# Kernel optimization log

Hardware: AMD Instinct MI355X
Metric: run time of the kernel (lower is better)

## Reference

```python
import jax, jax.numpy as jnp
import numpy as np

# Superlevel-set persistence (sublevel of f = -beta) on a Freudenthal-triangulated grid.
# dim-0 pairs: Kruskal union-find on vertices (edges ascending by lower-star value).
# dim-1 pairs: union-find on the dual graph (triangles + outer face, edges descending),
# valid because the grid complex is a planar disk (standard duality for 2-complexes).

def _find(parent, x):
    root = x
    while parent[root] != root:
        root = parent[root]
    while parent[x] != root:
        parent[x], x = root, parent[x]
    return root

def _persistence_pairs(beta_np):
    n0, n1 = beta_np.shape
    f = (-beta_np).reshape(-1)            # sublevel filtration of -beta == superlevel of beta
    N = n0 * n1
    idx = np.arange(N).reshape(n0, n1)
    # Freudenthal edges: horizontal, vertical, diagonal (i,j)-(i+1,j+1)
    eu = np.concatenate([idx[:, :-1].ravel(), idx[:-1, :].ravel(), idx[:-1, :-1].ravel()])
    ev = np.concatenate([idx[:, 1:].ravel(), idx[1:, :].ravel(), idx[1:, 1:].ravel()])
    e_crit = np.where(f[eu] >= f[ev], eu, ev)   # lower-star critical vertex of each edge
    e_val = f[e_crit]
    # ---- dim 0: union-find over vertices, edges ascending ----
    order = np.argsort(e_val, kind='stable')
    parent = np.arange(N)
    birth_vtx = np.arange(N)              # per-root: vertex of minimal f in component
    b0, d0 = [], []
    for e in order:
        ru, rv = _find(parent, eu[e]), _find(parent, ev[e])
        if ru == rv:
            continue
        if f[birth_vtx[ru]] < f[birth_vtx[rv]]:
            ru, rv = rv, ru               # ru = younger component (larger birth) dies
        b0.append(birth_vtx[ru]); d0.append(e_crit[e])
        parent[ru] = rv                   # surviving root keeps the older birth vertex
    # ---- triangles of the Freudenthal triangulation ----
    t_a = np.concatenate([idx[:-1, :-1].ravel(), idx[:-1, :-1].ravel()])
    t_b = np.concatenate([idx[1:, :-1].ravel(), idx[:-1, 1:].ravel()])
    t_c = np.concatenate([idx[1:, 1:].ravel(), idx[1:, 1:].ravel()])
    T = t_a.shape[0]
    tris = np.stack([t_a, t_b, t_c], 1)
    t_arg = np.argmax(np.stack([f[t_a], f[t_b], f[t_c]], 1), 1)
    t_crit = tris[np.arange(T), t_arg]    # lower-star critical vertex of each triangle
    # ---- dual graph: nodes = triangles + outer face, dual edges = primal edges ----
    edge2face = {}
    for t in range(T):
        vs = tris[t]
        for a, b in ((0, 1), (0, 2), (1, 2)):
            key = (min(vs[a], vs[b]), max(vs[a], vs[b]))
            edge2face.setdefault(key, []).append(t)
    OUTER = T
    du, dv, dval, dcrit = [], [], [], []
    for (a, b), faces in edge2face.items():
        du.append(faces[0]); dv.append(faces[1] if len(faces) > 1 else OUTER)
        c = a if f[a] >= f[b] else b
        dcrit.append(c); dval.append(f[c])
    du = np.array(du); dv = np.array(dv)
    dval = np.array(dval); dcrit = np.array(dcrit)
    # ---- dim 1: union-find over faces, dual edges descending ----
    order1 = np.argsort(-dval, kind='stable')
    parent1 = np.arange(T + 1)
    fval = np.concatenate([f[t_crit], [np.inf]])   # outer face value = +inf
    fcrit = np.concatenate([t_crit, [-1]])
    birth_face = np.arange(T + 1)         # per-root: face of maximal value in component
    be1, dt1 = [], []
    for e in order1:
        ru, rv = _find(parent1, du[e]), _find(parent1, dv[e])
        if ru == rv:
            continue
        if fval[birth_face[ru]] > fval[birth_face[rv]]:
            ru, rv = rv, ru               # ru = younger (smaller max face value)
        be1.append(dcrit[e])              # H1 birth: the merging primal edge
        dt1.append(fcrit[birth_face[ru]]) # H1 death: max triangle of younger component
        parent1[ru] = rv
    return (np.asarray(b0, np.int64), np.asarray(d0, np.int64),
            np.asarray(be1, np.int64), np.asarray(dt1, np.int64))


def setup_inputs() -> dict:
    key = jax.random.key(0)
    beta = jax.random.normal(key, (128, 128), dtype=jnp.float32)
    return {"beta": beta}


def reference(beta):
    b0, d0, be1, dt1 = _persistence_pairs(np.asarray(beta))
    bf = beta.reshape(-1)
    # dim-0 superlevel bar lengths: beta[birth_vtx] - beta[death_vtx]  (SumBarcodeLengths(dim=0))
    loss0 = jnp.sum(bf[b0] - bf[d0]) if b0.size else jnp.zeros((), bf.dtype)
    # dim-1 lengths: beta[edge_crit] - beta[tri_crit]; skip the single longest bar
    if be1.size:
        l1 = bf[be1] - bf[dt1]
        loss1 = jnp.sum(l1) - jnp.max(l1)  # PartialSumBarcodeLengths(dim=1, skip=1)
    else:
        loss1 = jnp.zeros((), bf.dtype)
    return loss1 + loss0
```

## Files before the change

### kernel.cpp

```cpp
#include <hip/hip_runtime.h>

#define NV 16384
#define EH 16256
#define EVV 16256
#define ED 16129
#define NE 48641
#define NT 32258
#define ND 32259
#define OUTERF 32258
#define TAILN 8192
#define FINT 1024

typedef unsigned int u32;
typedef unsigned short u16;

static __host__ __device__ constexpr size_t al256(size_t x) { return (x + 255) & ~(size_t)255; }
static constexpr size_t OFF_ACC   = 0;
static constexpr size_t OFF_R32   = 256;
static constexpr size_t OFF_FVAL  = OFF_R32   + al256(NV * 4);
static constexpr size_t OFF_CTV   = OFF_FVAL  + al256(ND * 4);
static constexpr size_t OFF_CNTR  = OFF_CTV   + al256(NT * 2);
static constexpr size_t OFF_FRK   = OFF_CNTR  + al256(NV * 4);
static constexpr size_t OFF_FRV   = OFF_FRK   + al256(ND * 4);
static constexpr size_t OFF_DVAL  = OFF_FRV   + al256(ND * 4);
static constexpr size_t OFF_WLA   = OFF_DVAL  + al256(NE * 4);
static constexpr size_t OFF_WLB   = OFF_WLA   + al256(NE * 8);
static constexpr size_t OFF_RTS   = OFF_WLB   + al256(NE * 8);
static constexpr size_t OFF_MTG   = OFF_RTS   + al256(NE * 4);
static constexpr size_t OFF_MTG2  = OFF_MTG   + al256((ND + 1) * 4);
static constexpr size_t OFF_PARG  = OFF_MTG2  + al256((ND + 1) * 4);

__device__ __forceinline__ u32 fmap(float x) {
  u32 u = __float_as_uint(x);
  return (u & 0x80000000u) ? ~u : (u | 0x80000000u);
}
__device__ __forceinline__ float funmap(u32 m) {
  u32 u = (m & 0x80000000u) ? (m & 0x7FFFFFFFu) : ~m;
  return __uint_as_float(u);
}

__device__ __forceinline__ int findh(volatile u16* par, int x) {
  while (true) {
    int p = par[x];
    if (p == x) return x;
    int gp = par[p];
    if (gp == p) return p;
    par[x] = (u16)gp;
    x = gp;
  }
}

__device__ __forceinline__ void decode_pe(u32 e, int& eu, int& ev) {
  if (e < EH) { int i = (int)(e / 127u), j = (int)(e - (u32)i * 127u); eu = (i << 7) + j; ev = eu + 1; }
  else if (e < EH + EVV) { int k = (int)(e - EH); eu = k; ev = k + 128; }
  else { int k = (int)(e - EH - EVV); int i = k / 127, j = k - i * 127; eu = (i << 7) + j; ev = eu + 129; }
}
__device__ __forceinline__ void decode_df(u32 e, int& fa, int& fb) {
  if (e < EH) { int i = (int)(e / 127u), j = (int)(e - (u32)i * 127u);
    fa = (i < 127) ? (ED + i * 127 + j) : OUTERF;
    fb = (i >= 1) ? ((i - 1) * 127 + j) : OUTERF; }
  else if (e < EH + EVV) { int k = (int)(e - EH); int i = k >> 7, j = k & 127;
    fa = (j < 127) ? (i * 127 + j) : OUTERF;
    fb = (j >= 1) ? (ED + i * 127 + (j - 1)) : OUTERF; }
  else { int k = (int)(e - EH - EVV); int i = k / 127, j = k - i * 127;
    fa = i * 127 + j; fb = ED + i * 127 + j; }
}

__global__ void k_init(float* accF, u32* r32, u32* mtabG, u32* mtabG2, u32* parG32) {
  int i = blockIdx.x * 256 + threadIdx.x;
  if (i < 12) accF[i] = 0.f;
  if (i < NV) r32[i] = 0u;
  if (i < (ND + 1) / 2) parG32[i] = ((2u * (u32)i + 1u) << 16) | (2u * (u32)i);
  if (i < ND + 1) { mtabG[i] = 0xFFFFFFFFu; mtabG2[i] = 0xFFFFFFFFu; }
}

__global__ void k_rankv(const float* __restrict__ beta, u32* r32) {
  int v = blockIdx.x * 256 + threadIdx.x;
  int c = blockIdx.y;
  float bv = beta[v];
  int u0 = c << 10;
  int cnt = 0;
#pragma unroll 8
  for (int u = u0; u < u0 + 1024; ++u) {
    float bu = beta[u];
    cnt += (bu < bv || (bu == bv && u < v)) ? 1 : 0;
  }
  if (cnt) atomicAdd(&r32[v], (u32)cnt);
}

__global__ void k_build(const float* __restrict__ beta, const u32* __restrict__ r32,
                        float* fval, u16* ctv, float* accF, u32* accU) {
  __shared__ float ls[4], lm[4];
  int bid = blockIdx.x, tid = threadIdx.x;
  if (bid < 64) {
    int v = (bid << 8) + tid;
    float b = beta[v];
    float s = b, m = b;
    for (int off = 32; off >= 1; off >>= 1) {
      s += __shfl_down(s, off);
      m = fmaxf(m, __shfl_down(m, off));
    }
    int wid = tid >> 6;
    if ((tid & 63) == 0) { ls[wid] = s; lm[wid] = m; }
    __syncthreads();
    if (tid == 0) {
      s = ls[0] + ls[1] + ls[2] + ls[3];
      m = fmaxf(fmaxf(lm[0], lm[1]), fmaxf(lm[2], lm[3]));
      atomicAdd(&accF[1], s);
      atomicMax(&accU[2], fmap(m));
    }
  } else {
    int t = ((bid - 64) << 8) + tid;
    float c = 0.f;
    if (t < NT) {
      int i, j, v0, v1, v2;
      if (t < ED) { i = t / 127; j = t - i * 127; v0 = (i << 7) + j; v1 = v0 + 128; v2 = v0 + 129; }
      else { int u = t - ED; i = u / 127; j = u - i * 127; v0 = (i << 7) + j; v1 = v0 + 1; v2 = v0 + 129; }
      u32 r0 = r32[v0], r1 = r32[v1], r2 = r32[v2];
      int crit = v0; u32 rm = r0;
      if (r1 < rm) { rm = r1; crit = v1; }
      if (r2 < rm) { rm = r2; crit = v2; }
      float fv = -beta[crit];
      fval[t] = fv;
      ctv[t] = (u16)crit;
      c = fv;
      if (t == 0) fval[OUTERF] = __builtin_inff();
    }
    for (int off = 32; off >= 1; off >>= 1) c += __shfl_down(c, off);
    int wid = tid >> 6;
    if ((tid & 63) == 0) ls[wid] = c;
    __syncthreads();
    if (tid == 0) atomicAdd(&accF[3], ls[0] + ls[1] + ls[2] + ls[3]);
  }
}

__global__ void k_cntface(const u16* __restrict__ ctv, const u32* __restrict__ r32, u32* cntR) {
  int v = blockIdx.x * 256 + threadIdx.x;
  int i = v >> 7, j = v & 127;
  int cnt = 0;
  if (i < 127 && j < 127) cnt += (ctv[i * 127 + j] == v);
  if (i >= 1 && j < 127)  cnt += (ctv[(i - 1) * 127 + j] == v);
  if (i >= 1 && j >= 1)   cnt += (ctv[(i - 1) * 127 + (j - 1)] == v);
  if (i < 127 && j < 127) cnt += (ctv[ED + i * 127 + j] == v);
  if (i < 127 && j >= 1)  cnt += (ctv[ED + i * 127 + (j - 1)] == v);
  if (i >= 1 && j >= 1)   cnt += (ctv[ED + (i - 1) * 127 + (j - 1)] == v);
  cntR[r32[v]] = (u32)cnt;
}

__global__ __launch_bounds__(1024) void k_scanR(u32* cntR) {
  __shared__ u32 wsum[16];
  int tid = threadIdx.x;
  u32 loc[16]; u32 s = 0;
#pragma unroll
  for (int k = 0; k < 16; ++k) { u32 c = cntR[(tid << 4) + k]; loc[k] = s; s += c; }
  int lane = tid & 63, wid = tid >> 6;
  u32 incl = s;
  for (int off = 1; off < 64; off <<= 1) {
    u32 o = __shfl_up(incl, off);
    if (lane >= off) incl += o;
  }
  if (lane == 63) wsum[wid] = incl;
  __syncthreads();
  u32 wbase = 0;
  for (int w = 0; w < wid; ++w) wbase += wsum[w];
  u32 base = wbase + incl - s + 1;
#pragma unroll
  for (int k = 0; k < 16; ++k) cntR[(tid << 4) + k] = base + loc[k];
}

__global__ void k_facerank(const u16* __restrict__ ctv, const u32* __restrict__ r32,
                           const u32* __restrict__ startsR, const float* __restrict__ fval,
                           u32* frk, float* frv) {
  int g = blockIdx.x * 256 + threadIdx.x;
  if (g == 0) { frk[OUTERF] = 0u; frv[0] = __builtin_inff(); }
  if (g >= NT) return;
  int v = ctv[g];
  int i = v >> 7, j = v & 127;
  int local = 0, f;
  if (i < 127 && j < 127) { f = i * 127 + j;             local += (f < g && ctv[f] == v); }
  if (i >= 1 && j < 127)  { f = (i - 1) * 127 + j;       local += (f < g && ctv[f] == v); }
  if (i >= 1 && j >= 1)   { f = (i - 1) * 127 + (j - 1); local += (f < g && ctv[f] == v); }
  if (i < 127 && j < 127) { f = ED + i * 127 + j;        local += (f < g && ctv[f] == v); }
  if (i < 127 && j >= 1)  { f = ED + i * 127 + (j - 1);  local += (f < g && ctv[f] == v); }
  if (i >= 1 && j >= 1)   { f = ED + (i - 1) * 127 + (j - 1); local += (f < g && ctv[f] == v); }
  u32 rk = startsR[r32[v]] + (u32)local;
  frk[g] = rk;
  frv[rk] = fval[g];
}

__global__ void k_edges(const float* __restrict__ beta, const u32* __restrict__ r32,
                        const u32* __restrict__ frk,
                        float* dvals, uint2* wl0, float* accF, u32* mtabG) {
  int e = blockIdx.x * 256 + threadIdx.x;
  float dv = 0.f;
  if (e < NE) {
    int eu, ev; decode_pe((u32)e, eu, ev);
    int fa, fb; decode_df((u32)e, fa, fb);
    u32 ru = r32[eu], rv = r32[ev];
    u32 rr = min(ru, rv);
    int cv = (ru <= rv) ? eu : ev;
    dv = -beta[cv];
    dvals[e] = dv;
    u32 ra = frk[fa], rb = frk[fb];
    u32 key = (rr << 17) | (u32)e;
    wl0[e] = make_uint2(ra | (rb << 16), key);
    atomicMin(&mtabG[ra], key);
    atomicMin(&mtabG[rb], key);
  }
  float ds = dv;
  for (int off = 32; off >= 1; off >>= 1) ds += __shfl_down(ds, off);
  if ((threadIdx.x & 63) == 0) atomicAdd(&accF[0], ds);
}

__global__ void k_win0(const uint2* __restrict__ wl0, const float* __restrict__ dvals,
                       const float* __restrict__ frv, const u32* __restrict__ mtabG,
                       u16* parG, uint2* owl, float* accF, u32* accU) {
  __shared__ float ls[4], lm[4];
  int tid = threadIdx.x, lane = tid & 63;
  int e = blockIdx.x * 256 + tid;
  float wDl = 0.f, lmx = 0.f;
  bool surv = false;
  uint2 rec = make_uint2(0u, 0u);
  if (e < NE) {
    rec = wl0[e];
    u32 a = rec.x & 0xFFFFu, b = rec.x >> 16;
    u32 y = max(a, b), o = min(a, b);
    if (mtabG[y] == rec.y) {
      parG[y] = (u16)o;
      float dv = dvals[rec.y & 0x1FFFFu];
      wDl = dv;
      lmx = frv[y] - dv;
    } else {
      surv = true;
    }
  }
  unsigned long long mk = __ballot(surv);
  int base = 0;
  if (lane == 0) {
    int c = __popcll(mk);
    if (c) base = (int)atomicAdd(&accU[6], (u32)c);
  }
  base = __shfl(base, 0);
  if (surv) owl[base + __popcll(mk & ((1ull << lane) - 1ull))] = rec;
  for (int off = 32; off >= 1; off >>= 1) {
    wDl += __shfl_down(wDl, off);
    lmx = fmaxf(lmx, __shfl_down(lmx, off));
  }
  if (lane == 0) { ls[tid >> 6] = wDl; lm[tid >> 6] = lmx; }
  __syncthreads();
  if (tid == 0) {
    float s = ls[0] + ls[1] + ls[2] + ls[3];
    float m = fmaxf(fmaxf(lm[0], lm[1]), fmaxf(lm[2], lm[3]));
    atomicAdd(&accF[4], s);
    atomicMax(&accU[5], fmap(m));
  }
}

__global__ void k_claimN(const uint2* __restrict__ wl, u16* parG, u32* rts,
                         u32* mtab, const u32* __restrict__ accU, int ci) {
  int n1 = (int)accU[ci];
  int i = blockIdx.x * 256 + threadIdx.x;
  if (i >= n1) return;
  uint2 rec = wl[i];
  int ra = findh((volatile u16*)parG, (int)(rec.x & 0xFFFFu));
  int rb = findh((volatile u16*)parG, (int)(rec.x >> 16));
  if (ra == rb) {
    rts[i] = 0xFFFFFFFFu;
  } else {
    rts[i] = (u32)ra | ((u32)rb << 16);
    atomicMin(&mtab[ra], rec.y);
    atomicMin(&mtab[rb], rec.y);
  }
}

__global__ void k_winN(const uint2* __restrict__ wl, const u32* __restrict__ rts,
                       const float* __restrict__ dvals, const float* __restrict__ frv,
                       const u32* __restrict__ mtab, u16* parG, uint2* owl,
                       float* accF, u32* accU, int ci, int co) {
  __shared__ float ls[4], lm[4];
  int tid = threadIdx.x, lane = tid & 63;
  int n1 = (int)accU[ci];
  int i = blockIdx.x * 256 + tid;
  bool active = i < n1;
  float wDl = 0.f, lmx = 0.f;
  bool surv = false;
  u32 pr = 0xFFFFFFFFu, key = 0;
  if (active) {
    key = wl[i].y;
    pr = rts[i];
  }
  if (active && pr != 0xFFFFFFFFu) {
    u32 a = pr & 0xFFFFu, b = pr >> 16;
    u32 y = max(a, b), o = min(a, b);
    if (mtab[y] == key) {
      parG[y] = (u16)o;
      float dv = dvals[key & 0x1FFFFu];
      wDl = dv;
      lmx = frv[y] - dv;
    } else {
      surv = true;
    }
  }
  unsigned long long mk = __ballot(surv);
  int base = 0;
  if (lane == 0) {
    int c = __popcll(mk);
    if (c) base = (int)atomicAdd(&accU[co], (u32)c);
  }
  base = __shfl(base, 0);
  if (surv) owl[base + __popcll(mk & ((1ull << lane) - 1ull))] = make_uint2(pr, key);
  for (int off = 32; off >= 1; off >>= 1) {
    wDl += __shfl_down(wDl, off);
    lmx = fmaxf(lmx, __shfl_down(lmx, off));
  }
  if (lane == 0) { ls[tid >> 6] = wDl; lm[tid >> 6] = lmx; }
  __syncthreads();
  if (tid == 0) {
    float s = ls[0] + ls[1] + ls[2] + ls[3];
    float m = fmaxf(fmaxf(lm[0], lm[1]), fmaxf(lm[2], lm[3]));
    atomicAdd(&accF[4], s);
    atomicMax(&accU[5], fmap(m));
  }
}

__global__ __launch_bounds__(1024) void k_dual(
    uint2* __restrict__ wlA, uint2* __restrict__ wlB, u32* __restrict__ rts,
    const u32* __restrict__ parG32, const float* __restrict__ dvals,
    const float* __restrict__ frv,
    const float* __restrict__ accF, const u32* __restrict__ accU, float* out) {
  __shared__ u16 par[ND + 1];
  __shared__ u32 pool[24576];
  __shared__ int nCur, nNxt;
  __shared__ int nTail[2];
  __shared__ float redS[16], redM[16];
  int tid = threadIdx.x, lane = tid & 63;
  {
    u32* p32 = (u32*)par;
    for (int v = tid; v < (ND + 1) / 2; v += 1024) p32[v] = parG32[v];
  }
  for (int h = tid; h < 16384; h += 1024) pool[h] = 0xFFFFFFFFu;
  if (tid == 0) { nNxt = 0; nTail[0] = 0; nTail[1] = 0; nCur = (int)accU[9]; }
  float wD = 0.f, lmax = 0.f;
  __syncthreads();
  uint2* cur = wlA;
  uint2* nxt = wlB;
  int n = nCur;
  for (int round = 0; round < 50000 && n > TAILN; ++round) {
    for (int i0 = 0; i0 < n; i0 += 1024) {
      int i = i0 + tid;
      if (i < n) {
        uint2 rec = cur[i];
        int ra = findh((volatile u16*)par, (int)(rec.x & 0xFFFFu));
        int rb = findh((volatile u16*)par, (int)(rec.x >> 16));
        if (ra == rb) {
          rts[i] = 0xFFFFFFFFu;
        } else {
          rts[i] = (u32)ra | ((u32)rb << 16);
          atomicMin(&pool[(u32)ra & 16383u], rec.y);
          atomicMin(&pool[(u32)rb & 16383u], rec.y);
        }
      }
    }
    __syncthreads();
    for (int i0 = 0; i0 < n; i0 += 1024) {
      int i = i0 + tid;
      bool active = i < n;
      u32 pr = 0xFFFFFFFFu, key = 0;
      if (active) {
        key = cur[i].y;
        pr = rts[i];
      }
      bool pend = active && (pr != 0xFFFFFFFFu);
      u32 y = 0, o = 0;
      bool win = false;
      if (pend) {
        u32 a = pr & 0xFFFFu, b = pr >> 16;
        y = max(a, b); o = min(a, b);
        win = (pool[y & 16383u] == key);
      }
      if (win) {
        par[y] = (u16)o;
        float dv = dvals[key & 0x1FFFFu];
        wD += dv;
        lmax = fmaxf(lmax, frv[y] - dv);
      }
      bool req = pend && !win;
      unsigned long long mk = __ballot(req);
      int base = 0;
      if (lane == 0) {
        int c = __popcll(mk);
        if (c) base = atomicAdd(&nNxt, c);
      }
      base = __shfl(base, 0);
      if (req) {
        int pos = base + __popcll(mk & ((1ull << lane) - 1ull));
        nxt[pos] = make_uint2(pr, key);
      }
    }
    __syncthreads();
    if (n <= 6144) {
      for (int i0 = 0; i0 < n; i0 += 1024) {
        int i = i0 + tid;
        if (i < n) {
          u32 pr = rts[i];
          if (pr != 0xFFFFFFFFu) {
            pool[(pr & 0xFFFFu) & 16383u] = 0xFFFFFFFFu;
            pool[(pr >> 16) & 16383u] = 0xFFFFFFFFu;
          }
        }
      }
    } else {
      for (int h = tid; h < 16384; h += 1024) pool[h] = 0xFFFFFFFFu;
    }
    for (int v = tid; v < ND; v += 1024) {
      int p = par[v]; int pp = par[p];
      if (p != pp) par[v] = (u16)pp;
    }
    if (tid == 0) { nCur = nNxt; nNxt = 0; }
    __syncthreads();
    n = nCur;
    uint2* s = cur; cur = nxt; nxt = s;
  }
  if (n > 0) {
    uint2* wlL = (uint2*)(pool + 8192);
    for (int i = tid; i < n; i += 1024) wlL[i] = cur[i];
    __syncthreads();
    int nL = n;
    int cb = 0;
    u32 oldp[8];
#pragma unroll
    for (int k = 0; k < 8; ++k) oldp[k] = 0xFFFFFFFFu;
    for (int sr = 0; sr < 100000; ++sr) {
      if (nL <= FINT) break;
      u32* mtC = pool + (cb << 12);
      u32* mtO = pool + ((cb ^ 1) << 12);
      u32 prc[8], keyr[8];
#pragma unroll
      for (int k = 0; k < 8; ++k) {
        if (oldp[k] != 0xFFFFFFFFu) {
          mtO[(oldp[k] & 0xFFFFu) & 4095u] = 0xFFFFFFFFu;
          mtO[(oldp[k] >> 16) & 4095u] = 0xFFFFFFFFu;
        }
        prc[k] = 0xFFFFFFFFu; keyr[k] = 0u;
        int i = tid + (k << 10);
        if (i < nL) {
          uint2 rec = wlL[i];
          int ra = findh((volatile u16*)par, (int)(rec.x & 0xFFFFu));
          int rb = findh((volatile u16*)par, (int)(rec.x >> 16));
          if (ra != rb) {
            u32 pr = (u32)ra | ((u32)rb << 16);
            prc[k] = pr; keyr[k] = rec.y;
            atomicMin(&mtC[(u32)ra & 4095u], rec.y);
            atomicMin(&mtC[(u32)rb & 4095u], rec.y);
          }
        }
      }
      if (tid == 0) nTail[cb] = 0;
      __syncthreads();
#pragma unroll
      for (int k = 0; k < 8; ++k) {
        bool surv = false;
        if (prc[k] != 0xFFFFFFFFu) {
          u32 a = prc[k] & 0xFFFFu, b = prc[k] >> 16;
          u32 y = max(a, b), o = min(a, b);
          if (mtC[y & 4095u] == keyr[k]) {
            par[y] = (u16)o;
            float dv = dvals[keyr[k] & 0x1FFFFu];
            wD += dv;
            lmax = fmaxf(lmax, frv[y] - dv);
          } else {
            surv = true;
          }
        }
        unsigned long long mk = __ballot(surv);
        int base = 0;
        if (lane == 0) {
          int c = __popcll(mk);
          if (c) base = atomicAdd(&nTail[cb], c);
        }
        base = __shfl(base, 0);
        if (surv) {
          int pos = base + __popcll(mk & ((1ull << lane) - 1ull));
          wlL[pos] = make_uint2(prc[k], keyr[k]);
        }
        oldp[k] = prc[k];
      }
      __syncthreads();
      nL = nTail[cb];
      cb ^= 1;
    }
    for (int h = tid; h < 8192; h += 1024) pool[h] = 0xFFFFFFFFu;
    __syncthreads();
    if (nL > 0 && tid < 64) {
      int m = nL;
      int mm = m;
      int guard = 0;
      while (mm > 0 && guard++ < 100000) {
        u32 prc[16];
        int resolved = 0;
#pragma unroll
        for (int k = 0; k < 16; ++k) {
          prc[k] = 0xFFFFFFFFu;
          int i = (k << 6) + lane;
          if (i < m) {
            uint2 rec = wlL[i];
            if (rec.x != 0xFFFFFFFFu) {
              int ra = findh((volatile u16*)par, (int)(rec.x & 0xFFFFu));
              int rb = findh((volatile u16*)par, (int)(rec.x >> 16));
              if (ra == rb) {
                wlL[i].x = 0xFFFFFFFFu;
                resolved++;
              } else {
                u32 pr = (u32)ra | ((u32)rb << 16);
                prc[k] = pr;
                wlL[i].x = pr;
                atomicMin(&pool[(u32)ra & 4095u], rec.y);
                atomicMin(&pool[(u32)rb & 4095u], rec.y);
              }
            }
          }
        }
        asm volatile("s_waitcnt lgkmcnt(0)" ::: "memory");
#pragma unroll
        for (int k = 0; k < 16; ++k) {
          if (prc[k] != 0xFFFFFFFFu) {
            int i = (k << 6) + lane;
            u32 key = wlL[i].y;
            u32 a = prc[k] & 0xFFFFu, b = prc[k] >> 16;
            u32 y = max(a, b), o = min(a, b);
            if (pool[y & 4095u] == key) {
              par[y] = (u16)o;
              float dv = dvals[key & 0x1FFFFu];
              wD += dv;
              lmax = fmaxf(lmax, frv[y] - dv);
              wlL[i].x = 0xFFFFFFFFu;
              resolved++;
            }
          }
        }
        asm volatile("s_waitcnt lgkmcnt(0)" ::: "memory");
#pragma unroll
        for (int k = 0; k < 16; ++k) {
          if (prc[k] != 0xFFFFFFFFu) {
            pool[(prc[k] & 0xFFFFu) & 4095u] = 0xFFFFFFFFu;
            pool[(prc[k] >> 16) & 4095u] = 0xFFFFFFFFu;
          }
        }
        asm volatile("s_waitcnt lgkmcnt(0)" ::: "memory");
        for (int off = 32; off >= 1; off >>= 1) resolved += __shfl_down(resolved, off);
        resolved = __shfl(resolved, 0);
        mm -= resolved;
      }
    }
  }
  __syncthreads();
  for (int off = 32; off >= 1; off >>= 1) {
    wD += __shfl_down(wD, off);
    lmax = fmaxf(lmax, __shfl_down(lmax, off));
  }
  if (lane == 0) { redS[tid >> 6] = wD; redM[tid >> 6] = lmax; }
  __syncthreads();
  if (tid == 0) {
    float s = 0.f, m = 0.f;
    for (int w = 0; w < 16; ++w) { s += redS[w]; m = fmaxf(m, redM[w]); }
    s += accF[4];
    m = fmaxf(m, funmap(accU[5]));
    float wmst = accF[0] - s;
    float loss0 = wmst + accF[1] - funmap(accU[2]);
    float sum1 = accF[3] - s;
    out[0] = loss0 + sum1 - m;
  }
}

extern "C" void kernel_launch(void* const* d_in, const int* in_sizes, int n_in,
                              void* d_out, int out_size, void* d_ws, size_t ws_size,
                              hipStream_t stream) {
  const float* beta = (const float*)d_in[0];
  float* out = (float*)d_out;
  char* ws = (char*)d_ws;
  float* accF = (float*)(ws + OFF_ACC);
  u32*   accU = (u32*)(ws + OFF_ACC);
  u32* r32 = (u32*)(ws + OFF_R32);
  float* fval = (float*)(ws + OFF_FVAL);
  u16* ctv = (u16*)(ws + OFF_CTV);
  u32* cntR = (u32*)(ws + OFF_CNTR);
  u32* frk = (u32*)(ws + OFF_FRK);
  float* frv = (float*)(ws + OFF_FRV);
  float* dvals = (float*)(ws + OFF_DVAL);
  uint2* wlA = (uint2*)(ws + OFF_WLA);
  uint2* wlB = (uint2*)(ws + OFF_WLB);
  u32* rts = (u32*)(ws + OFF_RTS);
  u32* mtabG = (u32*)(ws + OFF_MTG);
  u32* mtabG2 = (u32*)(ws + OFF_MTG2);
  u16* parG = (u16*)(ws + OFF_PARG);
  u32* parG32 = (u32*)(ws + OFF_PARG);

  hipLaunchKernelGGL(k_init, dim3(127), dim3(256), 0, stream, accF, r32, mtabG, mtabG2, parG32);
  hipLaunchKernelGGL(k_rankv, dim3(64, 16), dim3(256), 0, stream, beta, r32);
  hipLaunchKernelGGL(k_build, dim3(191), dim3(256), 0, stream, beta, r32, fval, ctv, accF, accU);
  hipLaunchKernelGGL(k_cntface, dim3(64), dim3(256), 0, stream, ctv, r32, cntR);
  hipLaunchKernelGGL(k_scanR, dim3(1), dim3(1024), 0, stream, cntR);
  hipLaunchKernelGGL(k_facerank, dim3(127), dim3(256), 0, stream, ctv, r32, cntR, fval, frk, frv);
  hipLaunchKernelGGL(k_edges, dim3(191), dim3(256), 0, stream, beta, r32, frk, dvals, wlA, accF, mtabG);
  hipLaunchKernelGGL(k_win0, dim3(191), dim3(256), 0, stream, wlA, dvals, frv, mtabG, parG, wlB, accF, accU);
  hipMemsetAsync(mtabG, 0xFF, (ND + 1) * sizeof(u32), stream);
  hipLaunchKernelGGL(k_claimN, dim3(191), dim3(256), 0, stream, wlB, parG, rts, mtabG2, accU, 6);
  hipLaunchKernelGGL(k_winN, dim3(191), dim3(256), 0, stream, wlB, rts, dvals, frv, mtabG2, parG, wlA, accF, accU, 6, 7);
  hipMemsetAsync(mtabG2, 0xFF, (ND + 1) * sizeof(u32), stream);
  hipLaunchKernelGGL(k_claimN, dim3(191), dim3(256), 0, stream, wlA, parG, rts, mtabG, accU, 7);
  hipLaunchKernelGGL(k_winN, dim3(191), dim3(256), 0, stream, wlA, rts, dvals, frv, mtabG, parG, wlB, accF, accU, 7, 8);
  hipLaunchKernelGGL(k_claimN, dim3(191), dim3(256), 0, stream, wlB, parG, rts, mtabG2, accU, 8);
  hipLaunchKernelGGL(k_winN, dim3(191), dim3(256), 0, stream, wlB, rts, dvals, frv, mtabG2, parG, wlA, accF, accU, 8, 9);
  hipLaunchKernelGGL(k_dual, dim3(1), dim3(1024), 0, stream, wlA, wlB, rts, parG32, dvals, frv, accF, accU, out);
}
```

Before: 257.5 us.

## Fuse mid-pipeline kernels into one cooperative kernel with grid syncs

Replaces the chain of about a dozen small launches and two memsets (build, face counting, scan, face ranking, edge setup, the initial win pass and three claim/win rounds) with a single cooperative kernel of 191 blocks that separates phases with grid.sync. The memsets of the min tables are replaced by targeted resets of only the entries touched in earlier rounds. A second rts buffer is added so consecutive rounds do not overwrite each other's data. This aims to remove per-launch overhead and inter-kernel gaps, at the cost of grid-barrier latency and a single-block scan that now handles 64 elements per thread.

```diff
diff --git a/kernel.cpp b/kernel.cpp
--- a/kernel.cpp
+++ b/kernel.cpp
@@ -1,4 +1,7 @@
 #include <hip/hip_runtime.h>
+#include <hip/hip_cooperative_groups.h>
+
+namespace cg = cooperative_groups;
 
 #define NV 16384
 #define EH 16256
@@ -26,7 +29,8 @@
 static constexpr size_t OFF_WLA   = OFF_DVAL  + al256(NE * 4);
 static constexpr size_t OFF_WLB   = OFF_WLA   + al256(NE * 8);
 static constexpr size_t OFF_RTS   = OFF_WLB   + al256(NE * 8);
-static constexpr size_t OFF_MTG   = OFF_RTS   + al256(NE * 4);
+static constexpr size_t OFF_RTS2  = OFF_RTS   + al256(NE * 4);
+static constexpr size_t OFF_MTG   = OFF_RTS2  + al256(NE * 4);
 static constexpr size_t OFF_MTG2  = OFF_MTG   + al256((ND + 1) * 4);
 static constexpr size_t OFF_PARG  = OFF_MTG2  + al256((ND + 1) * 4);
 
@@ -88,10 +92,18 @@
   if (cnt) atomicAdd(&r32[v], (u32)cnt);
 }
 
-__global__ void k_build(const float* __restrict__ beta, const u32* __restrict__ r32,
-                        float* fval, u16* ctv, float* accF, u32* accU) {
+__global__ __launch_bounds__(256) void k_coop(
+    const float* __restrict__ beta, const u32* __restrict__ r32,
+    float* accF, u32* accU,
+    float* fval, u16* ctv, u32* cntR, u32* frk, float* frv,
+    float* dvals, uint2* wlA, uint2* wlB, u32* rts, u32* rts2,
+    u32* mtabG, u32* mtabG2, u16* parG) {
+  cg::grid_group grid = cg::this_grid();
   __shared__ float ls[4], lm[4];
-  int bid = blockIdx.x, tid = threadIdx.x;
+  __shared__ u32 wsum[4];
+  int tid = threadIdx.x, lane = tid & 63, wid = tid >> 6;
+  int bid = blockIdx.x;
+  int gtid = bid * 256 + tid;
   if (bid < 64) {
     int v = (bid << 8) + tid;
     float b = beta[v];
@@ -100,8 +112,7 @@
       s += __shfl_down(s, off);
       m = fmaxf(m, __shfl_down(m, off));
     }
-    int wid = tid >> 6;
-    if ((tid & 63) == 0) { ls[wid] = s; lm[wid] = m; }
+    if (lane == 0) { ls[wid] = s; lm[wid] = m; }
     __syncthreads();
     if (tid == 0) {
       s = ls[0] + ls[1] + ls[2] + ls[3];
@@ -127,199 +138,199 @@
       if (t == 0) fval[OUTERF] = __builtin_inff();
     }
     for (int off = 32; off >= 1; off >>= 1) c += __shfl_down(c, off);
-    int wid = tid >> 6;
-    if ((tid & 63) == 0) ls[wid] = c;
+    if (lane == 0) ls[wid] = c;
     __syncthreads();
     if (tid == 0) atomicAdd(&accF[3], ls[0] + ls[1] + ls[2] + ls[3]);
   }
-}
-
-__global__ void k_cntface(const u16* __restrict__ ctv, const u32* __restrict__ r32, u32* cntR) {
-  int v = blockIdx.x * 256 + threadIdx.x;
-  int i = v >> 7, j = v & 127;
-  int cnt = 0;
-  if (i < 127 && j < 127) cnt += (ctv[i * 127 + j] == v);
-  if (i >= 1 && j < 127)  cnt += (ctv[(i - 1) * 127 + j] == v);
-  if (i >= 1 && j >= 1)   cnt += (ctv[(i - 1) * 127 + (j - 1)] == v);
-  if (i < 127 && j < 127) cnt += (ctv[ED + i * 127 + j] == v);
-  if (i < 127 && j >= 1)  cnt += (ctv[ED + i * 127 + (j - 1)] == v);
-  if (i >= 1 && j >= 1)   cnt += (ctv[ED + (i - 1) * 127 + (j - 1)] == v);
-  cntR[r32[v]] = (u32)cnt;
-}
-
-__global__ __launch_bounds__(1024) void k_scanR(u32* cntR) {
-  __shared__ u32 wsum[16];
-  int tid = threadIdx.x;
-  u32 loc[16]; u32 s = 0;
-#pragma unroll
-  for (int k = 0; k < 16; ++k) { u32 c = cntR[(tid << 4) + k]; loc[k] = s; s += c; }
-  int lane = tid & 63, wid = tid >> 6;
-  u32 incl = s;
-  for (int off = 1; off < 64; off <<= 1) {
-    u32 o = __shfl_up(incl, off);
-    if (lane >= off) incl += o;
-  }
-  if (lane == 63) wsum[wid] = incl;
-  __syncthreads();
-  u32 wbase = 0;
-  for (int w = 0; w < wid; ++w) wbase += wsum[w];
-  u32 base = wbase + incl - s + 1;
-#pragma unroll
-  for (int k = 0; k < 16; ++k) cntR[(tid << 4) + k] = base + loc[k];
-}
-
-__global__ void k_facerank(const u16* __restrict__ ctv, const u32* __restrict__ r32,
-                           const u32* __restrict__ startsR, const float* __restrict__ fval,
-                           u32* frk, float* frv) {
-  int g = blockIdx.x * 256 + threadIdx.x;
-  if (g == 0) { frk[OUTERF] = 0u; frv[0] = __builtin_inff(); }
-  if (g >= NT) return;
-  int v = ctv[g];
-  int i = v >> 7, j = v & 127;
-  int local = 0, f;
-  if (i < 127 && j < 127) { f = i * 127 + j;             local += (f < g && ctv[f] == v); }
-  if (i >= 1 && j < 127)  { f = (i - 1) * 127 + j;       local += (f < g && ctv[f] == v); }
-  if (i >= 1 && j >= 1)   { f = (i - 1) * 127 + (j - 1); local += (f < g && ctv[f] == v); }
-  if (i < 127 && j < 127) { f = ED + i * 127 + j;        local += (f < g && ctv[f] == v); }
-  if (i < 127 && j >= 1)  { f = ED + i * 127 + (j - 1);  local += (f < g && ctv[f] == v); }
-  if (i >= 1 && j >= 1)   { f = ED + (i - 1) * 127 + (j - 1); local += (f < g && ctv[f] == v); }
-  u32 rk = startsR[r32[v]] + (u32)local;
-  frk[g] = rk;
-  frv[rk] = fval[g];
-}
-
-__global__ void k_edges(const float* __restrict__ beta, const u32* __restrict__ r32,
-                        const u32* __restrict__ frk,
-                        float* dvals, uint2* wl0, float* accF, u32* mtabG) {
-  int e = blockIdx.x * 256 + threadIdx.x;
-  float dv = 0.f;
-  if (e < NE) {
-    int eu, ev; decode_pe((u32)e, eu, ev);
-    int fa, fb; decode_df((u32)e, fa, fb);
-    u32 ru = r32[eu], rv = r32[ev];
-    u32 rr = min(ru, rv);
-    int cv = (ru <= rv) ? eu : ev;
-    dv = -beta[cv];
-    dvals[e] = dv;
-    u32 ra = frk[fa], rb = frk[fb];
-    u32 key = (rr << 17) | (u32)e;
-    wl0[e] = make_uint2(ra | (rb << 16), key);
-    atomicMin(&mtabG[ra], key);
-    atomicMin(&mtabG[rb], key);
-  }
-  float ds = dv;
-  for (int off = 32; off >= 1; off >>= 1) ds += __shfl_down(ds, off);
-  if ((threadIdx.x & 63) == 0) atomicAdd(&accF[0], ds);
-}
-
-__global__ void k_win0(const uint2* __restrict__ wl0, const float* __restrict__ dvals,
-                       const float* __restrict__ frv, const u32* __restrict__ mtabG,
-                       u16* parG, uint2* owl, float* accF, u32* accU) {
-  __shared__ float ls[4], lm[4];
-  int tid = threadIdx.x, lane = tid & 63;
-  int e = blockIdx.x * 256 + tid;
-  float wDl = 0.f, lmx = 0.f;
-  bool surv = false;
-  uint2 rec = make_uint2(0u, 0u);
-  if (e < NE) {
-    rec = wl0[e];
-    u32 a = rec.x & 0xFFFFu, b = rec.x >> 16;
-    u32 y = max(a, b), o = min(a, b);
-    if (mtabG[y] == rec.y) {
-      parG[y] = (u16)o;
-      float dv = dvals[rec.y & 0x1FFFFu];
-      wDl = dv;
-      lmx = frv[y] - dv;
-    } else {
-      surv = true;
-    }
-  }
-  unsigned long long mk = __ballot(surv);
-  int base = 0;
-  if (lane == 0) {
-    int c = __popcll(mk);
-    if (c) base = (int)atomicAdd(&accU[6], (u32)c);
-  }
-  base = __shfl(base, 0);
-  if (surv) owl[base + __popcll(mk & ((1ull << lane) - 1ull))] = rec;
-  for (int off = 32; off >= 1; off >>= 1) {
-    wDl += __shfl_down(wDl, off);
-    lmx = fmaxf(lmx, __shfl_down(lmx, off));
-  }
-  if (lane == 0) { ls[tid >> 6] = wDl; lm[tid >> 6] = lmx; }
-  __syncthreads();
-  if (tid == 0) {
-    float s = ls[0] + ls[1] + ls[2] + ls[3];
-    float m = fmaxf(fmaxf(lm[0], lm[1]), fmaxf(lm[2], lm[3]));
-    atomicAdd(&accF[4], s);
-    atomicMax(&accU[5], fmap(m));
-  }
-}
-
-__global__ void k_claimN(const uint2* __restrict__ wl, u16* parG, u32* rts,
-                         u32* mtab, const u32* __restrict__ accU, int ci) {
-  int n1 = (int)accU[ci];
-  int i = blockIdx.x * 256 + threadIdx.x;
-  if (i >= n1) return;
-  uint2 rec = wl[i];
-  int ra = findh((volatile u16*)parG, (int)(rec.x & 0xFFFFu));
-  int rb = findh((volatile u16*)parG, (int)(rec.x >> 16));
-  if (ra == rb) {
-    rts[i] = 0xFFFFFFFFu;
-  } else {
-    rts[i] = (u32)ra | ((u32)rb << 16);
-    atomicMin(&mtab[ra], rec.y);
-    atomicMin(&mtab[rb], rec.y);
-  }
-}
-
-__global__ void k_winN(const uint2* __restrict__ wl, const u32* __restrict__ rts,
-                       const float* __restrict__ dvals, const float* __restrict__ frv,
-                       const u32* __restrict__ mtab, u16* parG, uint2* owl,
-                       float* accF, u32* accU, int ci, int co) {
-  __shared__ float ls[4], lm[4];
-  int tid = threadIdx.x, lane = tid & 63;
-  int n1 = (int)accU[ci];
-  int i = blockIdx.x * 256 + tid;
-  bool active = i < n1;
-  float wDl = 0.f, lmx = 0.f;
-  bool surv = false;
-  u32 pr = 0xFFFFFFFFu, key = 0;
-  if (active) {
-    key = wl[i].y;
-    pr = rts[i];
-  }
-  if (active && pr != 0xFFFFFFFFu) {
-    u32 a = pr & 0xFFFFu, b = pr >> 16;
-    u32 y = max(a, b), o = min(a, b);
-    if (mtab[y] == key) {
-      parG[y] = (u16)o;
-      float dv = dvals[key & 0x1FFFFu];
-      wDl = dv;
-      lmx = frv[y] - dv;
-    } else {
-      surv = true;
-    }
-  }
-  unsigned long long mk = __ballot(surv);
-  int base = 0;
-  if (lane == 0) {
-    int c = __popcll(mk);
-    if (c) base = (int)atomicAdd(&accU[co], (u32)c);
-  }
-  base = __shfl(base, 0);
-  if (surv) owl[base + __popcll(mk & ((1ull << lane) - 1ull))] = make_uint2(pr, key);
-  for (int off = 32; off >= 1; off >>= 1) {
-    wDl += __shfl_down(wDl, off);
-    lmx = fmaxf(lmx, __shfl_down(lmx, off));
-  }
-  if (lane == 0) { ls[tid >> 6] = wDl; lm[tid >> 6] = lmx; }
-  __syncthreads();
-  if (tid == 0) {
-    float s = ls[0] + ls[1] + ls[2] + ls[3];
-    float m = fmaxf(fmaxf(lm[0], lm[1]), fmaxf(lm[2], lm[3]));
-    atomicAdd(&accF[4], s);
-    atomicMax(&accU[5], fmap(m));
+  grid.sync();
+  if (gtid < NV) {
+    int v = gtid;
+    int i = v >> 7, j = v & 127;
+    int cnt = 0;
+    if (i < 127 && j < 127) cnt += (ctv[i * 127 + j] == v);
+    if (i >= 1 && j < 127)  cnt += (ctv[(i - 1) * 127 + j] == v);
+    if (i >= 1 && j >= 1)   cnt += (ctv[(i - 1) * 127 + (j - 1)] == v);
+    if (i < 127 && j < 127) cnt += (ctv[ED + i * 127 + j] == v);
+    if (i < 127 && j >= 1)  cnt += (ctv[ED + i * 127 + (j - 1)] == v);
+    if (i >= 1 && j >= 1)   cnt += (ctv[ED + (i - 1) * 127 + (j - 1)] == v);
+    cntR[r32[v]] = (u32)cnt;
+  }
+  grid.sync();
+  if (bid == 0) {
+    int b0 = tid << 6;
+    u32 s = 0;
+    for (int k = 0; k < 64; ++k) s += cntR[b0 + k];
+    u32 incl = s;
+    for (int off = 1; off < 64; off <<= 1) {
+      u32 o = __shfl_up(incl, off);
+      if (lane >= off) incl += o;
+    }
+    if (lane == 63) wsum[wid] = incl;
+    __syncthreads();
+    u32 wbase = 0;
+    for (int w = 0; w < wid; ++w) wbase += wsum[w];
+    u32 running = wbase + incl - s + 1;
+    for (int k = 0; k < 64; ++k) {
+      u32 c = cntR[b0 + k];
+      cntR[b0 + k] = running;
+      running += c;
+    }
+  }
+  grid.sync();
+  if (gtid == 0) { frk[OUTERF] = 0u; frv[0] = __builtin_inff(); }
+  if (gtid < NT) {
+    int g = gtid;
+    int v = ctv[g];
+    int i = v >> 7, j = v & 127;
+    int local = 0, f;
+    if (i < 127 && j < 127) { f = i * 127 + j;             local += (f < g && ctv[f] == v); }
+    if (i >= 1 && j < 127)  { f = (i - 1) * 127 + j;       local += (f < g && ctv[f] == v); }
+    if (i >= 1 && j >= 1)   { f = (i - 1) * 127 + (j - 1); local += (f < g && ctv[f] == v); }
+    if (i < 127 && j < 127) { f = ED + i * 127 + j;        local += (f < g && ctv[f] == v); }
+    if (i < 127 && j >= 1)  { f = ED + i * 127 + (j - 1);  local += (f < g && ctv[f] == v); }
+    if (i >= 1 && j >= 1)   { f = ED + (i - 1) * 127 + (j - 1); local += (f < g && ctv[f] == v); }
+    u32 rk = cntR[r32[v]] + (u32)local;
+    frk[g] = rk;
+    frv[rk] = fval[g];
+  }
+  grid.sync();
+  {
+    int e = gtid;
+    float dv = 0.f;
+    if (e < NE) {
+      int eu, ev; decode_pe((u32)e, eu, ev);
+      int fa, fb; decode_df((u32)e, fa, fb);
+      u32 ru = r32[eu], rv = r32[ev];
+      u32 rr = min(ru, rv);
+      int cv = (ru <= rv) ? eu : ev;
+      dv = -beta[cv];
+      dvals[e] = dv;
+      u32 ra = frk[fa], rb = frk[fb];
+      u32 key = (rr << 17) | (u32)e;
+      wlA[e] = make_uint2(ra | (rb << 16), key);
+      atomicMin(&mtabG[ra], key);
+      atomicMin(&mtabG[rb], key);
+    }
+    float ds = dv;
+    for (int off = 32; off >= 1; off >>= 1) ds += __shfl_down(ds, off);
+    if (lane == 0 && ds != 0.f) atomicAdd(&accF[0], ds);
+  }
+  grid.sync();
+  {
+    float wDl = 0.f, lmx = 0.f;
+    bool surv = false;
+    uint2 rec = make_uint2(0u, 0u);
+    if (gtid < NE) {
+      rec = wlA[gtid];
+      u32 a = rec.x & 0xFFFFu, b = rec.x >> 16;
+      u32 y = max(a, b), o = min(a, b);
+      if (mtabG[y] == rec.y) {
+        parG[y] = (u16)o;
+        float dv = dvals[rec.y & 0x1FFFFu];
+        wDl = dv;
+        lmx = frv[y] - dv;
+      } else {
+        surv = true;
+      }
+    }
+    unsigned long long mk = __ballot(surv);
+    int base = 0;
+    if (lane == 0) {
+      int c = __popcll(mk);
+      if (c) base = (int)atomicAdd(&accU[6], (u32)c);
+    }
+    base = __shfl(base, 0);
+    if (surv) wlB[base + __popcll(mk & ((1ull << lane) - 1ull))] = rec;
+    for (int off = 32; off >= 1; off >>= 1) {
+      wDl += __shfl_down(wDl, off);
+      lmx = fmaxf(lmx, __shfl_down(lmx, off));
+    }
+    if (lane == 0) { ls[wid] = wDl; lm[wid] = lmx; }
+    __syncthreads();
+    if (tid == 0) {
+      atomicAdd(&accF[4], ls[0] + ls[1] + ls[2] + ls[3]);
+      atomicMax(&accU[5], fmap(fmaxf(fmaxf(lm[0], lm[1]), fmaxf(lm[2], lm[3]))));
+    }
+  }
+  grid.sync();
+  for (int r = 1; r <= 3; ++r) {
+    u32* mt = (r & 1) ? mtabG2 : mtabG;
+    u32* rt = (r & 1) ? rts : rts2;
+    const uint2* inl = (r & 1) ? wlB : wlA;
+    uint2* outl = (r & 1) ? wlA : wlB;
+    int ci = 5 + r, co = 6 + r;
+    if (r == 2) {
+      int n1 = (int)accU[6];
+      if (gtid < n1) {
+        u32 pr = rts[gtid];
+        if (pr != 0xFFFFFFFFu) { mtabG2[pr & 0xFFFFu] = 0xFFFFFFFFu; mtabG2[pr >> 16] = 0xFFFFFFFFu; }
+      }
+    }
+    if (r == 1) {
+      if (gtid < NE) {
+        u32 x = wlA[gtid].x;
+        mtabG[x & 0xFFFFu] = 0xFFFFFFFFu;
+        mtabG[x >> 16] = 0xFFFFFFFFu;
+      }
+    }
+    {
+      int n1 = (int)accU[ci];
+      if (gtid < n1) {
+        uint2 rec = inl[gtid];
+        int ra = findh((volatile u16*)parG, (int)(rec.x & 0xFFFFu));
+        int rb = findh((volatile u16*)parG, (int)(rec.x >> 16));
+        if (ra == rb) {
+          rt[gtid] = 0xFFFFFFFFu;
+        } else {
+          rt[gtid] = (u32)ra | ((u32)rb << 16);
+          atomicMin(&mt[ra], rec.y);
+          atomicMin(&mt[rb], rec.y);
+        }
+      }
+    }
+    grid.sync();
+    {
+      int n1 = (int)accU[ci];
+      bool active = gtid < n1;
+      float wDl = 0.f, lmx = 0.f;
+      bool surv = false;
+      u32 pr = 0xFFFFFFFFu, key = 0;
+      if (active) {
+        key = inl[gtid].y;
+        pr = rt[gtid];
+      }
+      if (active && pr != 0xFFFFFFFFu) {
+        u32 a = pr & 0xFFFFu, b = pr >> 16;
+        u32 y = max(a, b), o = min(a, b);
+        if (mt[y] == key) {
+          parG[y] = (u16)o;
+          float dv = dvals[key & 0x1FFFFu];
+          wDl = dv;
+          lmx = frv[y] - dv;
+        } else {
+          surv = true;
+        }
+      }
+      unsigned long long mk = __ballot(surv);
+      int base = 0;
+      if (lane == 0) {
+        int c = __popcll(mk);
+        if (c) base = (int)atomicAdd(&accU[co], (u32)c);
+      }
+      base = __shfl(base, 0);
+      if (surv) outl[base + __popcll(mk & ((1ull << lane) - 1ull))] = make_uint2(pr, key);
+      for (int off = 32; off >= 1; off >>= 1) {
+        wDl += __shfl_down(wDl, off);
+        lmx = fmaxf(lmx, __shfl_down(lmx, off));
+      }
+      if (lane == 0) { ls[wid] = wDl; lm[wid] = lmx; }
+      __syncthreads();
+      if (tid == 0) {
+        atomicAdd(&accF[4], ls[0] + ls[1] + ls[2] + ls[3]);
+        atomicMax(&accU[5], fmap(fmaxf(fmaxf(lm[0], lm[1]), fmaxf(lm[2], lm[3]))));
+      }
+    }
+    grid.sync();
   }
 }
 
@@ -590,6 +601,7 @@
   uint2* wlA = (uint2*)(ws + OFF_WLA);
   uint2* wlB = (uint2*)(ws + OFF_WLB);
   u32* rts = (u32*)(ws + OFF_RTS);
+  u32* rts2 = (u32*)(ws + OFF_RTS2);
   u32* mtabG = (u32*)(ws + OFF_MTG);
   u32* mtabG2 = (u32*)(ws + OFF_MTG2);
   u16* parG = (u16*)(ws + OFF_PARG);
@@ -597,19 +609,10 @@
 
   hipLaunchKernelGGL(k_init, dim3(127), dim3(256), 0, stream, accF, r32, mtabG, mtabG2, parG32);
   hipLaunchKernelGGL(k_rankv, dim3(64, 16), dim3(256), 0, stream, beta, r32);
-  hipLaunchKernelGGL(k_build, dim3(191), dim3(256), 0, stream, beta, r32, fval, ctv, accF, accU);
-  hipLaunchKernelGGL(k_cntface, dim3(64), dim3(256), 0, stream, ctv, r32, cntR);
-  hipLaunchKernelGGL(k_scanR, dim3(1), dim3(1024), 0, stream, cntR);
-  hipLaunchKernelGGL(k_facerank, dim3(127), dim3(256), 0, stream, ctv, r32, cntR, fval, frk, frv);
-  hipLaunchKernelGGL(k_edges, dim3(191), dim3(256), 0, stream, beta, r32, frk, dvals, wlA, accF, mtabG);
-  hipLaunchKernelGGL(k_win0, dim3(191), dim3(256), 0, stream, wlA, dvals, frv, mtabG, parG, wlB, accF, accU);
-  hipMemsetAsync(mtabG, 0xFF, (ND + 1) * sizeof(u32), stream);
-  hipLaunchKernelGGL(k_claimN, dim3(191), dim3(256), 0, stream, wlB, parG, rts, mtabG2, accU, 6);
-  hipLaunchKernelGGL(k_winN, dim3(191), dim3(256), 0, stream, wlB, rts, dvals, frv, mtabG2, parG, wlA, accF, accU, 6, 7);
-  hipMemsetAsync(mtabG2, 0xFF, (ND + 1) * sizeof(u32), stream);
-  hipLaunchKernelGGL(k_claimN, dim3(191), dim3(256), 0, stream, wlA, parG, rts, mtabG, accU, 7);
-  hipLaunchKernelGGL(k_winN, dim3(191), dim3(256), 0, stream, wlA, rts, dvals, frv, mtabG, parG, wlB, accF, accU, 7, 8);
-  hipLaunchKernelGGL(k_claimN, dim3(191), dim3(256), 0, stream, wlB, parG, rts, mtabG2, accU, 8);
-  hipLaunchKernelGGL(k_winN, dim3(191), dim3(256), 0, stream, wlB, rts, dvals, frv, mtabG2, parG, wlA, accF, accU, 8, 9);
+  void* kargs[] = { (void*)&beta, (void*)&r32, (void*)&accF, (void*)&accU,
+                    (void*)&fval, (void*)&ctv, (void*)&cntR, (void*)&frk, (void*)&frv,
+                    (void*)&dvals, (void*)&wlA, (void*)&wlB, (void*)&rts, (void*)&rts2,
+                    (void*)&mtabG, (void*)&mtabG2, (void*)&parG };
+  hipLaunchCooperativeKernel((const void*)k_coop, dim3(191), dim3(256), kargs, 0, stream);
   hipLaunchKernelGGL(k_dual, dim3(1), dim3(1024), 0, stream, wlA, wlB, rts, parG32, dvals, frv, accF, accU, out);
 }
```

Result: slower. 451.5 us (+75.3%).

## Compact tail worklist each round and use fresh claim tables instead of memsets

Applied to the files above, without the earlier changes.

The single-wave tail loop in k_dual now loads records into registers, resolves them, and ballot-compacts the surviving edges back into the LDS worklist each iteration. Later rounds therefore scan only live entries instead of rescanning tombstoned slots, and the cross-lane reduction of the resolved count is gone. Separately, two extra claim tables are allocated and initialised in k_init, which removes the two hipMemsetAsync calls between Borůvka-style rounds. The cost is more register pressure, from 48 registers of record state per lane, plus extra workspace and init stores.

```diff
diff --git a/kernel.cpp b/kernel.cpp
--- a/kernel.cpp
+++ b/kernel.cpp
@@ -28,7 +28,9 @@
 static constexpr size_t OFF_RTS   = OFF_WLB   + al256(NE * 8);
 static constexpr size_t OFF_MTG   = OFF_RTS   + al256(NE * 4);
 static constexpr size_t OFF_MTG2  = OFF_MTG   + al256((ND + 1) * 4);
-static constexpr size_t OFF_PARG  = OFF_MTG2  + al256((ND + 1) * 4);
+static constexpr size_t OFF_MTG3  = OFF_MTG2  + al256((ND + 1) * 4);
+static constexpr size_t OFF_MTG4  = OFF_MTG3  + al256((ND + 1) * 4);
+static constexpr size_t OFF_PARG  = OFF_MTG4  + al256((ND + 1) * 4);
 
 __device__ __forceinline__ u32 fmap(float x) {
   u32 u = __float_as_uint(x);
@@ -66,12 +68,16 @@
     fa = i * 127 + j; fb = ED + i * 127 + j; }
 }
 
-__global__ void k_init(float* accF, u32* r32, u32* mtabG, u32* mtabG2, u32* parG32) {
+__global__ void k_init(float* accF, u32* r32, u32* mtabG, u32* mtabG2,
+                       u32* mtabG3, u32* mtabG4, u32* parG32) {
   int i = blockIdx.x * 256 + threadIdx.x;
   if (i < 12) accF[i] = 0.f;
   if (i < NV) r32[i] = 0u;
   if (i < (ND + 1) / 2) parG32[i] = ((2u * (u32)i + 1u) << 16) | (2u * (u32)i);
-  if (i < ND + 1) { mtabG[i] = 0xFFFFFFFFu; mtabG2[i] = 0xFFFFFFFFu; }
+  if (i < ND + 1) {
+    mtabG[i] = 0xFFFFFFFFu; mtabG2[i] = 0xFFFFFFFFu;
+    mtabG3[i] = 0xFFFFFFFFu; mtabG4[i] = 0xFFFFFFFFu;
+  }
 }
 
 __global__ void k_rankv(const float* __restrict__ beta, u32* r32) {
@@ -493,30 +499,28 @@
     __syncthreads();
     if (nL > 0 && tid < 64) {
       int m = nL;
-      int mm = m;
       int guard = 0;
-      while (mm > 0 && guard++ < 100000) {
-        u32 prc[16];
-        int resolved = 0;
+      while (m > 0 && guard++ < 100000) {
+        u32 rx[16], ry[16], prc[16];
+#pragma unroll
+        for (int k = 0; k < 16; ++k) {
+          int i = (k << 6) + lane;
+          rx[k] = 0xFFFFFFFFu; ry[k] = 0u;
+          if (i < m) { uint2 rec = wlL[i]; rx[k] = rec.x; ry[k] = rec.y; }
+        }
+        asm volatile("s_waitcnt lgkmcnt(0)" ::: "memory");
 #pragma unroll
         for (int k = 0; k < 16; ++k) {
           prc[k] = 0xFFFFFFFFu;
-          int i = (k << 6) + lane;
-          if (i < m) {
-            uint2 rec = wlL[i];
-            if (rec.x != 0xFFFFFFFFu) {
-              int ra = findh((volatile u16*)par, (int)(rec.x & 0xFFFFu));
-              int rb = findh((volatile u16*)par, (int)(rec.x >> 16));
-              if (ra == rb) {
-                wlL[i].x = 0xFFFFFFFFu;
-                resolved++;
-              } else {
-                u32 pr = (u32)ra | ((u32)rb << 16);
-                prc[k] = pr;
-                wlL[i].x = pr;
-                atomicMin(&pool[(u32)ra & 4095u], rec.y);
-                atomicMin(&pool[(u32)rb & 4095u], rec.y);
-              }
+          if (rx[k] != 0xFFFFFFFFu) {
+            int ra = findh((volatile u16*)par, (int)(rx[k] & 0xFFFFu));
+            int rb = findh((volatile u16*)par, (int)(rx[k] >> 16));
+            if (ra == rb) {
+              rx[k] = 0xFFFFFFFFu;
+            } else {
+              prc[k] = (u32)ra | ((u32)rb << 16);
+              atomicMin(&pool[(u32)ra & 4095u], ry[k]);
+              atomicMin(&pool[(u32)rb & 4095u], ry[k]);
             }
           }
         }
@@ -524,17 +528,14 @@
 #pragma unroll
         for (int k = 0; k < 16; ++k) {
           if (prc[k] != 0xFFFFFFFFu) {
-            int i = (k << 6) + lane;
-            u32 key = wlL[i].y;
             u32 a = prc[k] & 0xFFFFu, b = prc[k] >> 16;
             u32 y = max(a, b), o = min(a, b);
-            if (pool[y & 4095u] == key) {
+            if (pool[y & 4095u] == ry[k]) {
               par[y] = (u16)o;
-              float dv = dvals[key & 0x1FFFFu];
+              float dv = dvals[ry[k] & 0x1FFFFu];
               wD += dv;
               lmax = fmaxf(lmax, frv[y] - dv);
-              wlL[i].x = 0xFFFFFFFFu;
-              resolved++;
+              rx[k] = 0xFFFFFFFFu;
             }
           }
         }
@@ -546,10 +547,17 @@
             pool[(prc[k] >> 16) & 4095u] = 0xFFFFFFFFu;
           }
         }
+        int mnew = 0;
+#pragma unroll
+        for (int k = 0; k < 16; ++k) {
+          bool lv = (rx[k] != 0xFFFFFFFFu);
+          unsigned long long mk = __ballot(lv);
+          int pos = mnew + (int)__popcll(mk & ((1ull << lane) - 1ull));
+          if (lv) wlL[pos] = make_uint2(prc[k], ry[k]);
+          mnew += (int)__popcll(mk);
+        }
         asm volatile("s_waitcnt lgkmcnt(0)" ::: "memory");
-        for (int off = 32; off >= 1; off >>= 1) resolved += __shfl_down(resolved, off);
-        resolved = __shfl(resolved, 0);
-        mm -= resolved;
+        m = mnew;
       }
     }
   }
@@ -592,10 +600,12 @@
   u32* rts = (u32*)(ws + OFF_RTS);
   u32* mtabG = (u32*)(ws + OFF_MTG);
   u32* mtabG2 = (u32*)(ws + OFF_MTG2);
+  u32* mtabG3 = (u32*)(ws + OFF_MTG3);
+  u32* mtabG4 = (u32*)(ws + OFF_MTG4);
   u16* parG = (u16*)(ws + OFF_PARG);
   u32* parG32 = (u32*)(ws + OFF_PARG);
 
-  hipLaunchKernelGGL(k_init, dim3(127), dim3(256), 0, stream, accF, r32, mtabG, mtabG2, parG32);
+  hipLaunchKernelGGL(k_init, dim3(127), dim3(256), 0, stream, accF, r32, mtabG, mtabG2, mtabG3, mtabG4, parG32);
   hipLaunchKernelGGL(k_rankv, dim3(64, 16), dim3(256), 0, stream, beta, r32);
   hipLaunchKernelGGL(k_build, dim3(191), dim3(256), 0, stream, beta, r32, fval, ctv, accF, accU);
   hipLaunchKernelGGL(k_cntface, dim3(64), dim3(256), 0, stream, ctv, r32, cntR);
@@ -603,13 +613,11 @@
   hipLaunchKernelGGL(k_facerank, dim3(127), dim3(256), 0, stream, ctv, r32, cntR, fval, frk, frv);
   hipLaunchKernelGGL(k_edges, dim3(191), dim3(256), 0, stream, beta, r32, frk, dvals, wlA, accF, mtabG);
   hipLaunchKernelGGL(k_win0, dim3(191), dim3(256), 0, stream, wlA, dvals, frv, mtabG, parG, wlB, accF, accU);
-  hipMemsetAsync(mtabG, 0xFF, (ND + 1) * sizeof(u32), stream);
   hipLaunchKernelGGL(k_claimN, dim3(191), dim3(256), 0, stream, wlB, parG, rts, mtabG2, accU, 6);
   hipLaunchKernelGGL(k_winN, dim3(191), dim3(256), 0, stream, wlB, rts, dvals, frv, mtabG2, parG, wlA, accF, accU, 6, 7);
-  hipMemsetAsync(mtabG2, 0xFF, (ND + 1) * sizeof(u32), stream);
-  hipLaunchKernelGGL(k_claimN, dim3(191), dim3(256), 0, stream, wlA, parG, rts, mtabG, accU, 7);
-  hipLaunchKernelGGL(k_winN, dim3(191), dim3(256), 0, stream, wlA, rts, dvals, frv, mtabG, parG, wlB, accF, accU, 7, 8);
-  hipLaunchKernelGGL(k_claimN, dim3(191), dim3(256), 0, stream, wlB, parG, rts, mtabG2, accU, 8);
-  hipLaunchKernelGGL(k_winN, dim3(191), dim3(256), 0, stream, wlB, rts, dvals, frv, mtabG2, parG, wlA, accF, accU, 8, 9);
+  hipLaunchKernelGGL(k_claimN, dim3(191), dim3(256), 0, stream, wlA, parG, rts, mtabG3, accU, 7);
+  hipLaunchKernelGGL(k_winN, dim3(191), dim3(256), 0, stream, wlA, rts, dvals, frv, mtabG3, parG, wlB, accF, accU, 7, 8);
+  hipLaunchKernelGGL(k_claimN, dim3(191), dim3(256), 0, stream, wlB, parG, rts, mtabG4, accU, 8);
+  hipLaunchKernelGGL(k_winN, dim3(191), dim3(256), 0, stream, wlB, rts, dvals, frv, mtabG4, parG, wlA, accF, accU, 8, 9);
   hipLaunchKernelGGL(k_dual, dim3(1), dim3(1024), 0, stream, wlA, wlB, rts, parG32, dvals, frv, accF, accU, out);
 }
```

After: 250.8 us. 1.03x faster.
